# Optimization experiments

Hardware: AMD Instinct MI355X
Metric: run time of the kernel (lower is better)

## Reference

```python
import jax, jax.numpy as jnp
import numpy as np

N, DH, DK, FF = 2048, 256, 64, 32


def setup_inputs() -> dict:
    key = jax.random.key(0)
    ks = jax.random.split(key, 12)
    s = lambda d: 1.0 / np.sqrt(d).astype(np.float32)
    return {
        "x": jax.random.normal(ks[0], (1, N, DH), dtype=jnp.float32),
        "adj": (jax.random.uniform(ks[1], (N, N)) < 0.05).astype(jnp.float32),
        "dense": jax.random.uniform(ks[2], (N, N), dtype=jnp.float32),
        "Wq": jax.random.normal(ks[3], (DH, DK)) * s(DH),
        "bq": jnp.zeros((DK,), jnp.float32),
        "Wk": jax.random.normal(ks[4], (DH, DK)) * s(DH),
        "bk": jnp.zeros((DK,), jnp.float32),
        "Wv": jax.random.normal(ks[5], (DH, DH)) * s(DH),
        "bv": jnp.zeros((DH,), jnp.float32),
        "W1": jax.random.normal(ks[6], (3, FF)) * s(3),
        "b1": jnp.zeros((FF,), jnp.float32),
        "W2": jax.random.normal(ks[7], (FF, FF)) * s(FF),
        "b2": jnp.zeros((FF,), jnp.float32),
        "W3": jax.random.normal(ks[8], (FF, 1)) * s(FF),
        "b3": jnp.zeros((1,), jnp.float32),
    }


def reference(x, adj, dense, Wq, bq, Wk, bk, Wv, bv, W1, b1, W2, b2, W3, b3):
    # x: (1, n, dh). Original repeats x to (n, n, dh); here we exploit that
    # q[i, j] = Q(x_j), k[i, j] = K(x_i), v[i, j] = V(x_j) so no n^2*dh tensor
    # is materialized, while the math is identical.
    x0 = x[0]                      # (n, dh)
    q = x0 @ Wq + bq               # (n, dk), Q(x_j)
    k = x0 @ Wk + bk               # (n, dk), K(x_i)
    v = x0 @ Wv + bv               # (n, dh), V(x_j)
    # out[i, j] = <Q(x_j), K(x_i)>
    scores = k @ q.T               # (n, n)
    feats = jnp.stack((scores, adj, dense), axis=2)      # (n, n, 3)
    h = jax.nn.relu(feats @ W1 + b1)                     # (n, n, FF)
    h = jax.nn.relu(h @ W2 + b2)                         # (n, n, FF)
    focus = jax.nn.softmax((h @ W3 + b3)[..., 0], axis=1)  # (n, n)
    # feature[i] = sum_j focus[i, j] * V(x_j)
    feature = focus @ v            # (n, dh)
    return feature[None]           # (1, n, dh)
```

## Files before the change

### kernel.cpp

```cpp
#include <hip/hip_runtime.h>
#include <math.h>


#define NN  2048
#define DHH 256
#define DKK 64

typedef float    f32x4 __attribute__((ext_vector_type(4)));
typedef _Float16 f16x8 __attribute__((ext_vector_type(8)));
typedef _Float16 f16x4 __attribute__((ext_vector_type(4)));
typedef _Float16 f16x2 __attribute__((ext_vector_type(2)));
typedef int      i32x2 __attribute__((ext_vector_type(2)));

#define MFMA16(a, b, c) __builtin_amdgcn_mfma_f32_16x16x16f16((a), (b), (c), 0, 0, 0)
#define MFMA32(a, b, c) __builtin_amdgcn_mfma_f32_16x16x32_f16((a), (b), (c), 0, 0, 0)

__global__ __launch_bounds__(256) void k_qkv(
    const float* __restrict__ x,
    const float* __restrict__ Wq, const float* __restrict__ bq,
    const float* __restrict__ Wk, const float* __restrict__ bk,
    const float* __restrict__ Wv, const float* __restrict__ bv,
    _Float16* __restrict__ q16, _Float16* __restrict__ k16,
    _Float16* __restrict__ vT)
{
    __shared__ float As[32][64];
    __shared__ float Bs[32][64];
    __shared__ _Float16 Ts[64 * 72];

    const int t  = threadIdx.x;
    const int m0 = blockIdx.x * 64;
    const int yb = blockIdx.y;

    const float* W; const float* bias; int wld; int cw0;
    if (yb == 0)      { W = Wq; bias = bq; wld = 64;  cw0 = 0; }
    else if (yb == 1) { W = Wk; bias = bk; wld = 64;  cw0 = 0; }
    else              { W = Wv; bias = bv; wld = 256; cw0 = (yb - 2) * 64; }

    const int tx = t & 15, ty = t >> 4;
    float acc[4][4] = {};

    for (int k0 = 0; k0 < DHH; k0 += 32) {
        {
            const int rr = t >> 3;
            const int cc = (t & 7) * 4;
            float4 a0 = *(const float4*)(x + (size_t)(m0 + rr)      * DHH + k0 + cc);
            float4 a1 = *(const float4*)(x + (size_t)(m0 + rr + 32) * DHH + k0 + cc);
            As[cc+0][rr]    = a0.x; As[cc+1][rr]    = a0.y; As[cc+2][rr]    = a0.z; As[cc+3][rr]    = a0.w;
            As[cc+0][rr+32] = a1.x; As[cc+1][rr+32] = a1.y; As[cc+2][rr+32] = a1.z; As[cc+3][rr+32] = a1.w;
        }
        {
            const int bk_ = t >> 4;
            const int bc  = (t & 15) * 4;
            *(float4*)&Bs[bk_][bc]      = *(const float4*)(W + (size_t)(k0 + bk_)      * wld + cw0 + bc);
            *(float4*)&Bs[bk_ + 16][bc] = *(const float4*)(W + (size_t)(k0 + bk_ + 16) * wld + cw0 + bc);
        }
        __syncthreads();
        #pragma unroll
        for (int kk = 0; kk < 32; ++kk) {
            float4 a = *(const float4*)&As[kk][ty * 4];
            float4 b = *(const float4*)&Bs[kk][tx * 4];
            float av[4] = {a.x, a.y, a.z, a.w};
            float bw[4] = {b.x, b.y, b.z, b.w};
            #pragma unroll
            for (int ii = 0; ii < 4; ++ii)
                #pragma unroll
                for (int jj = 0; jj < 4; ++jj)
                    acc[ii][jj] = fmaf(av[ii], bw[jj], acc[ii][jj]);
        }
        __syncthreads();
    }

    float4 b4 = *(const float4*)&bias[cw0 + tx * 4];
    float bc4[4] = {b4.x, b4.y, b4.z, b4.w};

    if (yb < 2) {
        _Float16* outp = (yb == 0) ? q16 : k16;
        #pragma unroll
        for (int ii = 0; ii < 4; ++ii) {
            f16x4 hv;
            #pragma unroll
            for (int jj = 0; jj < 4; ++jj) hv[jj] = (_Float16)(acc[ii][jj] + bc4[jj]);
            *(f16x4*)&outp[(size_t)(m0 + ty * 4 + ii) * 64 + tx * 4] = hv;
        }
    } else {
        #pragma unroll
        for (int jj = 0; jj < 4; ++jj) {
            f16x4 hv;
            #pragma unroll
            for (int ii = 0; ii < 4; ++ii) hv[ii] = (_Float16)(acc[ii][jj] + bc4[jj]);
            *(f16x4*)&Ts[(tx * 4 + jj) * 72 + ty * 4] = hv;
        }
        __syncthreads();
        {
            const int c = t >> 2, seg = t & 3;
            f16x8 r0 = *(const f16x8*)&Ts[c * 72 + seg * 16];
            f16x8 r1 = *(const f16x8*)&Ts[c * 72 + seg * 16 + 8];
            *(f16x8*)&vT[(size_t)(cw0 + c) * NN + m0 + seg * 16]     = r0;
            *(f16x8*)&vT[(size_t)(cw0 + c) * NN + m0 + seg * 16 + 8] = r1;
        }
    }
}

__global__ __launch_bounds__(256) void k_mlp(
    const _Float16* __restrict__ q16, const _Float16* __restrict__ k16,
    const float* __restrict__ adj, const float* __restrict__ dense,
    const float* __restrict__ W1, const float* __restrict__ b1,
    const float* __restrict__ W2, const float* __restrict__ b2,
    const float* __restrict__ W3,
    _Float16* __restrict__ focus)
{
    __shared__ float red[8];

    const int t    = threadIdx.x;
    const int lane = t & 63;
    const int w    = t >> 6;
    const int col  = lane & 15;
    const int q    = lane >> 4;
    const int i    = blockIdx.x;

    const f16x8 kA0 = *(const f16x8*)&k16[(size_t)i * 64 + q * 8];
    const f16x8 kA1 = *(const f16x8*)&k16[(size_t)i * 64 + 32 + q * 8];

    f16x4 l1A0 = {}, l1A1 = {};
    {
        const float w0a = W1[col], w0b = W1[col + 16];
        const _Float16 h0a = (_Float16)w0a, h0b = (_Float16)w0b;
        if (q == 0) {
            l1A0[0] = h0a; l1A0[1] = h0a;
            l1A0[2] = (_Float16)W1[32 + col];
            l1A0[3] = (_Float16)W1[64 + col];
            l1A1[0] = h0b; l1A1[1] = h0b;
            l1A1[2] = (_Float16)W1[32 + col + 16];
            l1A1[3] = (_Float16)W1[64 + col + 16];
        } else if (q == 1) {
            l1A0[0] = (_Float16)(w0a - (float)h0a);
            l1A1[0] = (_Float16)(w0b - (float)h0b);
        }
    }

    f16x4 w2A[2][2];
    #pragma unroll
    for (int fh = 0; fh < 2; ++fh)
        #pragma unroll
        for (int oh = 0; oh < 2; ++oh)
            #pragma unroll
            for (int j = 0; j < 4; ++j)
                w2A[fh][oh][j] = (_Float16)W2[(fh * 16 + q * 4 + j) * 32 + oh * 16 + col];

    f32x4 c1a, c1b, c2a, c2b, w3v, w3v2;
    #pragma unroll
    for (int r = 0; r < 4; ++r) {
        c1a[r]  = b1[q * 4 + r];
        c1b[r]  = b1[16 + q * 4 + r];
        c2a[r]  = b2[q * 4 + r];
        c2b[r]  = b2[16 + q * 4 + r];
        w3v[r]  = W3[q * 4 + r];
        w3v2[r] = W3[16 + q * 4 + r];
    }

    const float* arow = adj   + (size_t)i * NN;
    const float* drow = dense + (size_t)i * NN;

    const f32x4 zero4 = {0.f, 0.f, 0.f, 0.f};
    float lg[8];

    for (int c = 0; c < 8; ++c) {
        const int base = w * 512 + c * 64;
        const int jj   = base + lane;

        const int u_ad = __builtin_bit_cast(int,
            __builtin_amdgcn_cvt_pkrtz(arow[jj], drow[jj]));

        float lgc = 0.f;
        #pragma unroll
        for (int st = 0; st < 4; ++st) {
            const int edge = base + st * 16 + col;

            f16x8 Qb0 = *(const f16x8*)&q16[(size_t)edge * 64 + q * 8];
            f16x8 Qb1 = *(const f16x8*)&q16[(size_t)edge * 64 + 32 + q * 8];
            f32x4 sC = MFMA32(kA0, Qb0, zero4);
            sC = MFMA32(kA1, Qb1, sC);
            const float s = sC[0];

            const _Float16 shi = (_Float16)s;
            _Float16 slo = (_Float16)(s - (float)shi);
            if (q == 1) slo = (_Float16)0;
            f16x2 r0; r0[0] = shi; r0[1] = slo;
            const int ad = __shfl(u_ad, st * 16 + col, 64);
            i32x2 b1v = { __builtin_bit_cast(int, r0), ad };
            f16x4 B1 = __builtin_bit_cast(f16x4, b1v);

            f32x4 hpA = MFMA16(l1A0, B1, c1a);
            f32x4 hpB = MFMA16(l1A1, B1, c1b);

            i32x2 p0 = { __builtin_bit_cast(int, __builtin_amdgcn_cvt_pkrtz(fmaxf(hpA[0], 0.f), fmaxf(hpA[1], 0.f))),
                         __builtin_bit_cast(int, __builtin_amdgcn_cvt_pkrtz(fmaxf(hpA[2], 0.f), fmaxf(hpA[3], 0.f))) };
            i32x2 p1 = { __builtin_bit_cast(int, __builtin_amdgcn_cvt_pkrtz(fmaxf(hpB[0], 0.f), fmaxf(hpB[1], 0.f))),
                         __builtin_bit_cast(int, __builtin_amdgcn_cvt_pkrtz(fmaxf(hpB[2], 0.f), fmaxf(hpB[3], 0.f))) };
            f16x4 B2f0 = __builtin_bit_cast(f16x4, p0);
            f16x4 B2f1 = __builtin_bit_cast(f16x4, p1);

            f32x4 acc0 = MFMA16(w2A[0][0], B2f0, c2a);
            acc0 = MFMA16(w2A[1][0], B2f1, acc0);
            f32x4 acc1 = MFMA16(w2A[0][1], B2f0, c2b);
            acc1 = MFMA16(w2A[1][1], B2f1, acc1);

            float p = 0.f;
            #pragma unroll
            for (int r = 0; r < 4; ++r) {
                p = fmaf(fmaxf(acc0[r], 0.f), w3v[r],  p);
                p = fmaf(fmaxf(acc1[r], 0.f), w3v2[r], p);
            }
            p += __shfl_xor(p, 16, 64);
            p += __shfl_xor(p, 32, 64);
            lgc = (q == st) ? p : lgc;
        }
        lg[c] = lgc;
    }

    float lmax = -1e30f;
    #pragma unroll
    for (int u = 0; u < 8; ++u) lmax = fmaxf(lmax, lg[u]);
    #pragma unroll
    for (int off = 32; off > 0; off >>= 1)
        lmax = fmaxf(lmax, __shfl_xor(lmax, off, 64));
    if (lane == 0) red[w] = lmax;
    __syncthreads();
    const float rmax = fmaxf(fmaxf(red[0], red[1]), fmaxf(red[2], red[3]));

    float lsum = 0.f;
    #pragma unroll
    for (int u = 0; u < 8; ++u) { lg[u] = __expf(lg[u] - rmax); lsum += lg[u]; }
    #pragma unroll
    for (int off = 32; off > 0; off >>= 1)
        lsum += __shfl_xor(lsum, off, 64);
    if (lane == 0) red[4 + w] = lsum;
    __syncthreads();
    const float inv = 1.f / (red[4] + red[5] + red[6] + red[7]);

    _Float16* hrow = focus + (size_t)i * NN;
    const int eb = w * 512 + q * 16 + col;
    #pragma unroll
    for (int u = 0; u < 8; ++u)
        hrow[eb + u * 64] = (_Float16)(lg[u] * inv);
}

__global__ __launch_bounds__(256) void k_feat(
    const _Float16* __restrict__ focus, const _Float16* __restrict__ vT,
    float* __restrict__ out)
{
    __shared__ float rbuf[3][64][8];

    const int t    = threadIdx.x;
    const int lane = t & 63;
    const int w    = t >> 6;
    const int col  = lane & 15;
    const int q    = lane >> 4;

    const int m0 = blockIdx.y * 16;
    const int n0 = blockIdx.x * 32;

    f32x4 acc0 = {}, acc1 = {};

    const size_t arow  = (size_t)(m0 + col) * NN;
    const size_t brow0 = (size_t)(n0 + col) * NN;
    const size_t brow1 = (size_t)(n0 + 16 + col) * NN;
    const int kb = w * 512 + q * 8;

    #pragma unroll 4
    for (int k0 = 0; k0 < 512; k0 += 32) {
        const int ko = kb + k0;
        f16x8 a  = *(const f16x8*)&focus[arow + ko];
        f16x8 b0 = *(const f16x8*)&vT[brow0 + ko];
        f16x8 b1 = *(const f16x8*)&vT[brow1 + ko];
        acc0 = MFMA32(a, b0, acc0);
        acc1 = MFMA32(a, b1, acc1);
    }

    if (w != 0) {
        *(float4*)&rbuf[w - 1][lane][0] = *(float4*)&acc0;
        *(float4*)&rbuf[w - 1][lane][4] = *(float4*)&acc1;
    }
    __syncthreads();

    if (w == 0) {
        #pragma unroll
        for (int j = 0; j < 3; ++j) {
            float4 p0 = *(const float4*)&rbuf[j][lane][0];
            float4 p1 = *(const float4*)&rbuf[j][lane][4];
            acc0[0] += p0.x; acc0[1] += p0.y; acc0[2] += p0.z; acc0[3] += p0.w;
            acc1[0] += p1.x; acc1[1] += p1.y; acc1[2] += p1.z; acc1[3] += p1.w;
        }
        #pragma unroll
        for (int r = 0; r < 4; ++r) {
            out[(size_t)(m0 + q * 4 + r) * DHH + n0 + col]      = acc0[r];
            out[(size_t)(m0 + q * 4 + r) * DHH + n0 + 16 + col] = acc1[r];
        }
    }
}

extern "C" void kernel_launch(void* const* d_in, const int* in_sizes, int n_in,
                              void* d_out, int out_size, void* d_ws, size_t ws_size,
                              hipStream_t stream) {
    const float* x     = (const float*)d_in[0];
    const float* adj   = (const float*)d_in[1];
    const float* dense = (const float*)d_in[2];
    const float* Wq    = (const float*)d_in[3];
    const float* bq    = (const float*)d_in[4];
    const float* Wk    = (const float*)d_in[5];
    const float* bk    = (const float*)d_in[6];
    const float* Wv    = (const float*)d_in[7];
    const float* bv    = (const float*)d_in[8];
    const float* W1    = (const float*)d_in[9];
    const float* b1    = (const float*)d_in[10];
    const float* W2    = (const float*)d_in[11];
    const float* b2    = (const float*)d_in[12];
    const float* W3    = (const float*)d_in[13];
    float* out = (float*)d_out;

    char* wsb = (char*)d_ws;
    _Float16* q16   = (_Float16*)(wsb);
    _Float16* k16   = (_Float16*)(wsb + 262144);
    _Float16* vT    = (_Float16*)(wsb + 524288);
    _Float16* focus = (_Float16*)(wsb + 1572864);

    hipLaunchKernelGGL(k_qkv,  dim3(32, 6),  dim3(256), 0, stream,
                       x, Wq, bq, Wk, bk, Wv, bv, q16, k16, vT);
    hipLaunchKernelGGL(k_mlp,  dim3(2048),   dim3(256), 0, stream,
                       q16, k16, adj, dense, W1, b1, W2, b2, W3, focus);
    hipLaunchKernelGGL(k_feat, dim3(8, 128), dim3(256), 0, stream,
                       focus, vT, out);
}
```

Baseline: 203.0 us.

## Precompute scores in a separate tiled MFMA kernel and use MFMA for layer-3 reduction

Moves the k·q score computation out of the per-row MLP kernel into a dedicated tiled GEMM kernel that writes hi/lo fp16 split scores to a 2048x2048 workspace. Focus is written in place over the score buffer with a doubled row stride. The MLP kernel now only loads those precomputed scores. It also replaces the final FF->1 projection (FMA loop plus two cross-lane shuffles) with two MFMA instructions. This trades redundant per-row tiny MFMAs for an extra 16 MB of global write and read traffic and a fourth kernel launch.

```diff
diff --git a/kernel.cpp b/kernel.cpp
--- a/kernel.cpp
+++ b/kernel.cpp
@@ -101,8 +101,52 @@
     }
 }
 
+__global__ __launch_bounds__(256) void k_scores(
+    const _Float16* __restrict__ q16, const _Float16* __restrict__ k16,
+    f16x2* __restrict__ schl)
+{
+    const int t    = threadIdx.x;
+    const int lane = t & 63;
+    const int w    = t >> 6;
+    const int col  = lane & 15;
+    const int q    = lane >> 4;
+
+    const int i0 = blockIdx.y * 128 + (w >> 1) * 64;
+    const int j0 = blockIdx.x * 128 + (w & 1) * 64;
+
+    f32x4 acc[4][4] = {};
+
+    #pragma unroll
+    for (int ks = 0; ks < 2; ++ks) {
+        f16x8 a[4], b[4];
+        #pragma unroll
+        for (int f = 0; f < 4; ++f) {
+            a[f] = *(const f16x8*)&k16[(size_t)(i0 + f * 16 + col) * 64 + ks * 32 + q * 8];
+            b[f] = *(const f16x8*)&q16[(size_t)(j0 + f * 16 + col) * 64 + ks * 32 + q * 8];
+        }
+        #pragma unroll
+        for (int fm = 0; fm < 4; ++fm)
+            #pragma unroll
+            for (int fn = 0; fn < 4; ++fn)
+                acc[fm][fn] = MFMA32(a[fm], b[fn], acc[fm][fn]);
+    }
+
+    #pragma unroll
+    for (int fm = 0; fm < 4; ++fm)
+        #pragma unroll
+        for (int fn = 0; fn < 4; ++fn)
+            #pragma unroll
+            for (int r = 0; r < 4; ++r) {
+                const size_t idx = (size_t)(i0 + fm * 16 + q * 4 + r) * NN + j0 + fn * 16 + col;
+                const float val = acc[fm][fn][r];
+                const _Float16 h = (_Float16)val;
+                f16x2 pk; pk[0] = h; pk[1] = (_Float16)(val - (float)h);
+                schl[idx] = pk;
+            }
+}
+
 __global__ __launch_bounds__(256) void k_mlp(
-    const _Float16* __restrict__ q16, const _Float16* __restrict__ k16,
+    const f16x2* __restrict__ schl,
     const float* __restrict__ adj, const float* __restrict__ dense,
     const float* __restrict__ W1, const float* __restrict__ b1,
     const float* __restrict__ W2, const float* __restrict__ b2,
@@ -117,9 +161,6 @@
     const int col  = lane & 15;
     const int q    = lane >> 4;
     const int i    = blockIdx.x;
-
-    const f16x8 kA0 = *(const f16x8*)&k16[(size_t)i * 64 + q * 8];
-    const f16x8 kA1 = *(const f16x8*)&k16[(size_t)i * 64 + 32 + q * 8];
 
     f16x4 l1A0 = {}, l1A1 = {};
     {
@@ -147,17 +188,23 @@
             for (int j = 0; j < 4; ++j)
                 w2A[fh][oh][j] = (_Float16)W2[(fh * 16 + q * 4 + j) * 32 + oh * 16 + col];
 
-    f32x4 c1a, c1b, c2a, c2b, w3v, w3v2;
+    f16x4 a3lo, a3hi;
+    #pragma unroll
+    for (int j = 0; j < 4; ++j) {
+        a3lo[j] = (_Float16)W3[q * 4 + j];
+        a3hi[j] = (_Float16)W3[16 + q * 4 + j];
+    }
+
+    f32x4 c1a, c1b, c2a, c2b;
     #pragma unroll
     for (int r = 0; r < 4; ++r) {
-        c1a[r]  = b1[q * 4 + r];
-        c1b[r]  = b1[16 + q * 4 + r];
-        c2a[r]  = b2[q * 4 + r];
-        c2b[r]  = b2[16 + q * 4 + r];
-        w3v[r]  = W3[q * 4 + r];
-        w3v2[r] = W3[16 + q * 4 + r];
-    }
-
+        c1a[r] = b1[q * 4 + r];
+        c1b[r] = b1[16 + q * 4 + r];
+        c2a[r] = b2[q * 4 + r];
+        c2b[r] = b2[16 + q * 4 + r];
+    }
+
+    const f16x2* srow = schl  + (size_t)i * NN;
     const float* arow = adj   + (size_t)i * NN;
     const float* drow = dense + (size_t)i * NN;
 
@@ -166,28 +213,18 @@
 
     for (int c = 0; c < 8; ++c) {
         const int base = w * 512 + c * 64;
-        const int jj   = base + lane;
-
-        const int u_ad = __builtin_bit_cast(int,
-            __builtin_amdgcn_cvt_pkrtz(arow[jj], drow[jj]));
-
         float lgc = 0.f;
         #pragma unroll
         for (int st = 0; st < 4; ++st) {
-            const int edge = base + st * 16 + col;
-
-            f16x8 Qb0 = *(const f16x8*)&q16[(size_t)edge * 64 + q * 8];
-            f16x8 Qb1 = *(const f16x8*)&q16[(size_t)edge * 64 + 32 + q * 8];
-            f32x4 sC = MFMA32(kA0, Qb0, zero4);
-            sC = MFMA32(kA1, Qb1, sC);
-            const float s = sC[0];
-
-            const _Float16 shi = (_Float16)s;
-            _Float16 slo = (_Float16)(s - (float)shi);
-            if (q == 1) slo = (_Float16)0;
-            f16x2 r0; r0[0] = shi; r0[1] = slo;
-            const int ad = __shfl(u_ad, st * 16 + col, 64);
-            i32x2 b1v = { __builtin_bit_cast(int, r0), ad };
+            const int e = base + st * 16 + col;
+
+            const int d0 = __builtin_bit_cast(int, srow[e]);
+            const int d1 = __builtin_bit_cast(int,
+                __builtin_amdgcn_cvt_pkrtz(arow[e], drow[e]));
+
+            const int m0 = (q == 0) ? d0 : ((q == 1) ? (d0 & 0xFFFF) : 0);
+            const int m1 = (q == 0) ? d1 : 0;
+            i32x2 b1v = {m0, m1};
             f16x4 B1 = __builtin_bit_cast(f16x4, b1v);
 
             f32x4 hpA = MFMA16(l1A0, B1, c1a);
@@ -205,15 +242,16 @@
             f32x4 acc1 = MFMA16(w2A[0][1], B2f0, c2b);
             acc1 = MFMA16(w2A[1][1], B2f1, acc1);
 
-            float p = 0.f;
-            #pragma unroll
-            for (int r = 0; r < 4; ++r) {
-                p = fmaf(fmaxf(acc0[r], 0.f), w3v[r],  p);
-                p = fmaf(fmaxf(acc1[r], 0.f), w3v2[r], p);
-            }
-            p += __shfl_xor(p, 16, 64);
-            p += __shfl_xor(p, 32, 64);
-            lgc = (q == st) ? p : lgc;
+            i32x2 p3a = { __builtin_bit_cast(int, __builtin_amdgcn_cvt_pkrtz(fmaxf(acc0[0], 0.f), fmaxf(acc0[1], 0.f))),
+                          __builtin_bit_cast(int, __builtin_amdgcn_cvt_pkrtz(fmaxf(acc0[2], 0.f), fmaxf(acc0[3], 0.f))) };
+            i32x2 p3b = { __builtin_bit_cast(int, __builtin_amdgcn_cvt_pkrtz(fmaxf(acc1[0], 0.f), fmaxf(acc1[1], 0.f))),
+                          __builtin_bit_cast(int, __builtin_amdgcn_cvt_pkrtz(fmaxf(acc1[2], 0.f), fmaxf(acc1[3], 0.f))) };
+            f16x4 B3f0 = __builtin_bit_cast(f16x4, p3a);
+            f16x4 B3f1 = __builtin_bit_cast(f16x4, p3b);
+
+            f32x4 c3 = MFMA16(a3lo, B3f0, zero4);
+            c3 = MFMA16(a3hi, B3f1, c3);
+            lgc = (q == st) ? c3[0] : lgc;
         }
         lg[c] = lgc;
     }
@@ -238,7 +276,7 @@
     __syncthreads();
     const float inv = 1.f / (red[4] + red[5] + red[6] + red[7]);
 
-    _Float16* hrow = focus + (size_t)i * NN;
+    _Float16* hrow = focus + (size_t)i * 2 * NN;
     const int eb = w * 512 + q * 16 + col;
     #pragma unroll
     for (int u = 0; u < 8; ++u)
@@ -262,7 +300,7 @@
 
     f32x4 acc0 = {}, acc1 = {};
 
-    const size_t arow  = (size_t)(m0 + col) * NN;
+    const size_t arow  = (size_t)(m0 + col) * (2 * NN);
     const size_t brow0 = (size_t)(n0 + col) * NN;
     const size_t brow1 = (size_t)(n0 + 16 + col) * NN;
     const int kb = w * 512 + q * 8;
@@ -322,12 +360,14 @@
     _Float16* q16   = (_Float16*)(wsb);
     _Float16* k16   = (_Float16*)(wsb + 262144);
     _Float16* vT    = (_Float16*)(wsb + 524288);
+    f16x2*    schl  = (f16x2*)   (wsb + 1572864);
     _Float16* focus = (_Float16*)(wsb + 1572864);
 
-    hipLaunchKernelGGL(k_qkv,  dim3(32, 6),  dim3(256), 0, stream,
+    hipLaunchKernelGGL(k_qkv,    dim3(32, 6),  dim3(256), 0, stream,
                        x, Wq, bq, Wk, bk, Wv, bv, q16, k16, vT);
-    hipLaunchKernelGGL(k_mlp,  dim3(2048),   dim3(256), 0, stream,
-                       q16, k16, adj, dense, W1, b1, W2, b2, W3, focus);
-    hipLaunchKernelGGL(k_feat, dim3(8, 128), dim3(256), 0, stream,
+    hipLaunchKernelGGL(k_scores, dim3(16, 16), dim3(256), 0, stream, q16, k16, schl);
+    hipLaunchKernelGGL(k_mlp,    dim3(2048),   dim3(256), 0, stream,
+                       schl, adj, dense, W1, b1, W2, b2, W3, focus);
+    hipLaunchKernelGGL(k_feat,   dim3(8, 128), dim3(256), 0, stream,
                        focus, vT, out);
 }
```

New measurement: 189.5 us. -6.7%, faster.
